# Performance work log

Measured on AMD Instinct MI355X. Metric: run time of the kernel, lower is better.

## Reference

```python
import jax, jax.numpy as jnp
import numpy as np

EPS = 1e-06

def phi(x):
    # canonical linear-attention feature map: elu(x) + 1 (positive features)
    return jax.nn.elu(x) + 1.0

def setup_inputs() -> dict:
    key = jax.random.key(0)
    kq, kk, kv = jax.random.split(key, 3)
    B, H, S, D = 4, 16, 4096, 64
    query = jax.random.normal(kq, (B, H, S, D), dtype=jnp.float32)
    k = jax.random.normal(kk, (B, H, S, D), dtype=jnp.float32)
    value = jax.random.normal(kv, (B, H, S, D), dtype=jnp.float32)
    attention_mask = jnp.ones((B, S), dtype=jnp.float32)
    return {"query": query, "key": k, "value": value, "attention_mask": attention_mask}

def reference(query, key, value, attention_mask):
    B, H, S, D = query.shape
    q = query / jnp.sqrt(jnp.asarray(D, query.dtype))
    phi_q = phi(q)                                   # [b,h,n,d]
    phi_k = phi(key)                                 # [b,h,n,d]
    mask = attention_mask[:, None, :, None].astype(phi_k.dtype)  # [b,1,n,1]
    phi_k = phi_k * mask
    kv_term = jnp.einsum('bhnd,bhnv->bhdv', phi_k, value)        # [b,h,d,v]
    output = jnp.einsum('bhnd,bhdv->bhnv', phi_q, kv_term)       # [b,h,n,v]
    k_one = jnp.sum(phi_k, axis=2)                               # [b,h,d] == phi_k @ masked ones
    normalizer = jnp.einsum('bhnd,bhd->bhn', phi_q, k_one)[..., None]  # [b,h,n,1]
    return output / (normalizer + EPS)
```

## Files before the change

kernel.cpp:

```cpp
#include <hip/hip_runtime.h>

#define NB 4
#define NH 16
#define NS 4096
#define ND 64
#define NBH (NB * NH)
#define EPSF 1e-6f

__device__ __forceinline__ float phi_f(float x) {
    return x > 0.0f ? x + 1.0f : __expf(x);
}

#define P1_CHUNK 512
#define P1_SUB 64

__global__ __launch_bounds__(256)
void la_pass1(const float* __restrict__ Kin, const float* __restrict__ Vin,
              const float* __restrict__ Min, float* __restrict__ KV,
              float* __restrict__ K1)
{
    const int tid = threadIdx.x;
    const int bh  = blockIdx.y;
    const int bb  = bh >> 4;
    const long long base = (long long)bh * NS * ND;
    const float* Kb = Kin + base;
    const float* Vb = Vin + base;
    const float* Mb = Min + (long long)bb * NS;

    __shared__ float sk[P1_SUB][ND];
    __shared__ float sv[P1_SUB][ND];

    const int lrow = tid >> 4;
    const int lcol = (tid & 15) * 4;
    const int d0 = (tid >> 4) * 4;
    const int v0 = (tid & 15) * 4;

    float acc[4][4];
    #pragma unroll
    for (int i = 0; i < 4; ++i)
        #pragma unroll
        for (int j = 0; j < 4; ++j) acc[i][j] = 0.0f;
    float acc1[4] = {0.f, 0.f, 0.f, 0.f};

    const int s0 = blockIdx.x * P1_CHUNK;
    const bool do_k1 = ((tid & 15) == 0);

    for (int t = 0; t < P1_CHUNK; t += P1_SUB) {
        __syncthreads();
        #pragma unroll
        for (int it = 0; it < 4; ++it) {
            const int r = lrow + 16 * it;
            const int srow = s0 + t + r;
            const float4 kq = *(const float4*)(Kb + (long long)srow * ND + lcol);
            const float4 vq = *(const float4*)(Vb + (long long)srow * ND + lcol);
            const float m = Mb[srow];
            float4 pk;
            pk.x = phi_f(kq.x) * m;
            pk.y = phi_f(kq.y) * m;
            pk.z = phi_f(kq.z) * m;
            pk.w = phi_f(kq.w) * m;
            *(float4*)(&sk[r][lcol]) = pk;
            *(float4*)(&sv[r][lcol]) = vq;
        }
        __syncthreads();
        #pragma unroll 4
        for (int r = 0; r < P1_SUB; ++r) {
            const float4 ka = *(const float4*)(&sk[r][d0]);
            const float4 vb = *(const float4*)(&sv[r][v0]);
            const float kav[4] = {ka.x, ka.y, ka.z, ka.w};
            const float vbv[4] = {vb.x, vb.y, vb.z, vb.w};
            #pragma unroll
            for (int i = 0; i < 4; ++i)
                #pragma unroll
                for (int j = 0; j < 4; ++j)
                    acc[i][j] += kav[i] * vbv[j];
            if (do_k1) {
                #pragma unroll
                for (int i = 0; i < 4; ++i) acc1[i] += kav[i];
            }
        }
    }

    float* kvb = KV + (long long)bh * ND * ND;
    #pragma unroll
    for (int i = 0; i < 4; ++i)
        #pragma unroll
        for (int j = 0; j < 4; ++j)
            atomicAdd(&kvb[(d0 + i) * ND + (v0 + j)], acc[i][j]);
    if (do_k1) {
        float* k1b = K1 + bh * ND;
        #pragma unroll
        for (int i = 0; i < 4; ++i) atomicAdd(&k1b[d0 + i], acc1[i]);
    }
}

#define P2_ROWS 128

__global__ __launch_bounds__(256)
void la_pass2(const float* __restrict__ Qin, const float* __restrict__ KV,
              const float* __restrict__ K1, float* __restrict__ Out)
{
    const int tid = threadIdx.x;
    const int bh  = blockIdx.y;
    const int s0  = blockIdx.x * P2_ROWS;
    const long long base = (long long)bh * NS * ND;

    __shared__ float sq[P2_ROWS][ND + 1];
    __shared__ float skv[ND][ND];
    __shared__ float sk1[ND];
    __shared__ float snorm[P2_ROWS];

    {
        const float4* kvsrc = (const float4*)(KV + (long long)bh * ND * ND);
        float4* kvdst = (float4*)(&skv[0][0]);
        #pragma unroll
        for (int i = 0; i < 4; ++i) kvdst[tid + 256 * i] = kvsrc[tid + 256 * i];
        if (tid < 16) ((float4*)sk1)[tid] = ((const float4*)(K1 + bh * ND))[tid];
    }

    {
        const int lrow = tid >> 4;
        const int lcol = (tid & 15) * 4;
        const float scale = 0.125f;
        #pragma unroll
        for (int it = 0; it < 8; ++it) {
            const int r = lrow + 16 * it;
            const float4 q4 = *(const float4*)(Qin + base + (long long)(s0 + r) * ND + lcol);
            sq[r][lcol + 0] = phi_f(q4.x * scale);
            sq[r][lcol + 1] = phi_f(q4.y * scale);
            sq[r][lcol + 2] = phi_f(q4.z * scale);
            sq[r][lcol + 3] = phi_f(q4.w * scale);
        }
    }
    __syncthreads();

    if (tid < P2_ROWS) {
        float n = 0.0f;
        #pragma unroll 8
        for (int d = 0; d < ND; ++d) n += sq[tid][d] * sk1[d];
        snorm[tid] = n;
    }
    __syncthreads();

    const int sg = tid >> 3;
    const int v0 = (tid & 7) * 8;
    const int r0 = sg * 4;

    float acc[4][8];
    #pragma unroll
    for (int j = 0; j < 4; ++j)
        #pragma unroll
        for (int k = 0; k < 8; ++k) acc[j][k] = 0.0f;

    #pragma unroll 4
    for (int d = 0; d < ND; ++d) {
        float q[4];
        #pragma unroll
        for (int j = 0; j < 4; ++j) q[j] = sq[r0 + j][d];
        const float4 b0 = *(const float4*)(&skv[d][v0]);
        const float4 b1 = *(const float4*)(&skv[d][v0 + 4]);
        const float bv[8] = {b0.x, b0.y, b0.z, b0.w, b1.x, b1.y, b1.z, b1.w};
        #pragma unroll
        for (int j = 0; j < 4; ++j)
            #pragma unroll
            for (int k = 0; k < 8; ++k)
                acc[j][k] += q[j] * bv[k];
    }

    float* outb = Out + base;
    #pragma unroll
    for (int j = 0; j < 4; ++j) {
        const int r = r0 + j;
        const float rn = 1.0f / (snorm[r] + EPSF);
        float4 o0, o1;
        o0.x = acc[j][0] * rn; o0.y = acc[j][1] * rn;
        o0.z = acc[j][2] * rn; o0.w = acc[j][3] * rn;
        o1.x = acc[j][4] * rn; o1.y = acc[j][5] * rn;
        o1.z = acc[j][6] * rn; o1.w = acc[j][7] * rn;
        *(float4*)(outb + (long long)(s0 + r) * ND + v0)     = o0;
        *(float4*)(outb + (long long)(s0 + r) * ND + v0 + 4) = o1;
    }
}

extern "C" void kernel_launch(void* const* d_in, const int* in_sizes, int n_in,
                              void* d_out, int out_size, void* d_ws, size_t ws_size,
                              hipStream_t stream)
{
    const float* Q = (const float*)d_in[0];
    const float* K = (const float*)d_in[1];
    const float* V = (const float*)d_in[2];
    const float* M = (const float*)d_in[3];
    float* Out = (float*)d_out;

    float* KV = (float*)d_ws;
    float* K1 = KV + (size_t)NBH * ND * ND;

    const size_t zbytes = ((size_t)NBH * ND * ND + (size_t)NBH * ND) * sizeof(float);
    hipMemsetAsync(d_ws, 0, zbytes, stream);

    dim3 g1(NS / P1_CHUNK, NBH);
    la_pass1<<<g1, dim3(256), 0, stream>>>(K, V, M, KV, K1);

    dim3 g2(NS / P2_ROWS, NBH);
    la_pass2<<<g2, dim3(256), 0, stream>>>(Q, KV, K1, Out);
}
```

Baseline: 256.4 us.

## Use single-wavefront blocks with 8x8 register tiles and register-prefetched loads

Both passes now run 64-thread blocks, one wavefront each, and every thread computes an 8x8 output tile instead of 4x4 or 4x8, which raises arithmetic per shared-memory load. Pass 1 uses smaller chunks and prefetches the next tile of K, V and the mask into registers while the current tile is being computed. Pass 2 transposes phi(Q) into shared memory so it can be read as float4, and it folds the normalizer dot product into the main loop. The trade-offs are many more blocks and many more atomics in pass 1, plus higher register pressure.

```diff
diff --git a/kernel.cpp b/kernel.cpp
--- a/kernel.cpp
+++ b/kernel.cpp
@@ -11,174 +11,220 @@
     return x > 0.0f ? x + 1.0f : __expf(x);
 }
 
-#define P1_CHUNK 512
-#define P1_SUB 64
-
-__global__ __launch_bounds__(256)
+#define P1_TILE 32
+#define P1_CHUNK 128
+
+__global__ __launch_bounds__(64)
 void la_pass1(const float* __restrict__ Kin, const float* __restrict__ Vin,
               const float* __restrict__ Min, float* __restrict__ KV,
               float* __restrict__ K1)
 {
-    const int tid = threadIdx.x;
-    const int bh  = blockIdx.y;
-    const int bb  = bh >> 4;
+    const int t  = threadIdx.x;
+    const int bh = blockIdx.y;
+    const int bb = bh >> 4;
     const long long base = (long long)bh * NS * ND;
     const float* Kb = Kin + base;
     const float* Vb = Vin + base;
     const float* Mb = Min + (long long)bb * NS;
 
-    __shared__ float sk[P1_SUB][ND];
-    __shared__ float sv[P1_SUB][ND];
-
-    const int lrow = tid >> 4;
-    const int lcol = (tid & 15) * 4;
-    const int d0 = (tid >> 4) * 4;
-    const int v0 = (tid & 15) * 4;
-
-    float acc[4][4];
-    #pragma unroll
-    for (int i = 0; i < 4; ++i)
-        #pragma unroll
-        for (int j = 0; j < 4; ++j) acc[i][j] = 0.0f;
-    float acc1[4] = {0.f, 0.f, 0.f, 0.f};
+    __shared__ float sk[P1_TILE * ND];
+    __shared__ float sv[P1_TILE * ND];
+
+    const int d0 = (t >> 3) * 8;
+    const int v0 = (t & 7) * 8;
+
+    float acc[8][8];
+    #pragma unroll
+    for (int i = 0; i < 8; ++i)
+        #pragma unroll
+        for (int j = 0; j < 8; ++j) acc[i][j] = 0.0f;
+    float acc1[8];
+    #pragma unroll
+    for (int i = 0; i < 8; ++i) acc1[i] = 0.0f;
 
     const int s0 = blockIdx.x * P1_CHUNK;
-    const bool do_k1 = ((tid & 15) == 0);
-
-    for (int t = 0; t < P1_CHUNK; t += P1_SUB) {
-        __syncthreads();
-        #pragma unroll
-        for (int it = 0; it < 4; ++it) {
-            const int r = lrow + 16 * it;
-            const int srow = s0 + t + r;
-            const float4 kq = *(const float4*)(Kb + (long long)srow * ND + lcol);
-            const float4 vq = *(const float4*)(Vb + (long long)srow * ND + lcol);
-            const float m = Mb[srow];
+
+    float4 kreg[8], vreg[8];
+    float  mreg[8];
+    #pragma unroll
+    for (int i = 0; i < 8; ++i) {
+        const int f = t + 64 * i;
+        const int r = f >> 4;
+        const int c = (f & 15) * 4;
+        const long long gr = (long long)(s0 + r) * ND + c;
+        kreg[i] = *(const float4*)(Kb + gr);
+        vreg[i] = *(const float4*)(Vb + gr);
+        mreg[i] = Mb[s0 + r];
+    }
+
+    for (int tile = 0; tile < P1_CHUNK / P1_TILE; ++tile) {
+        __syncthreads();
+        const int nt0 = s0 + (tile + 1) * P1_TILE;
+        #pragma unroll
+        for (int i = 0; i < 8; ++i) {
+            const int f = t + 64 * i;
             float4 pk;
-            pk.x = phi_f(kq.x) * m;
-            pk.y = phi_f(kq.y) * m;
-            pk.z = phi_f(kq.z) * m;
-            pk.w = phi_f(kq.w) * m;
-            *(float4*)(&sk[r][lcol]) = pk;
-            *(float4*)(&sv[r][lcol]) = vq;
+            pk.x = phi_f(kreg[i].x) * mreg[i];
+            pk.y = phi_f(kreg[i].y) * mreg[i];
+            pk.z = phi_f(kreg[i].z) * mreg[i];
+            pk.w = phi_f(kreg[i].w) * mreg[i];
+            *(float4*)(sk + f * 4) = pk;
+            *(float4*)(sv + f * 4) = vreg[i];
+            if (tile < P1_CHUNK / P1_TILE - 1) {
+                const int r = f >> 4;
+                const int c = (f & 15) * 4;
+                const long long gr = (long long)(nt0 + r) * ND + c;
+                kreg[i] = *(const float4*)(Kb + gr);
+                vreg[i] = *(const float4*)(Vb + gr);
+                mreg[i] = Mb[nt0 + r];
+            }
         }
         __syncthreads();
         #pragma unroll 4
-        for (int r = 0; r < P1_SUB; ++r) {
-            const float4 ka = *(const float4*)(&sk[r][d0]);
-            const float4 vb = *(const float4*)(&sv[r][v0]);
-            const float kav[4] = {ka.x, ka.y, ka.z, ka.w};
-            const float vbv[4] = {vb.x, vb.y, vb.z, vb.w};
+        for (int r = 0; r < P1_TILE; ++r) {
+            const float4 a0 = *(const float4*)(sk + r * ND + d0);
+            const float4 a1 = *(const float4*)(sk + r * ND + d0 + 4);
+            const float4 b0 = *(const float4*)(sv + r * ND + v0);
+            const float4 b1 = *(const float4*)(sv + r * ND + v0 + 4);
+            const float av[8] = {a0.x, a0.y, a0.z, a0.w, a1.x, a1.y, a1.z, a1.w};
+            const float bv[8] = {b0.x, b0.y, b0.z, b0.w, b1.x, b1.y, b1.z, b1.w};
             #pragma unroll
-            for (int i = 0; i < 4; ++i)
+            for (int i = 0; i < 8; ++i) {
+                acc1[i] += av[i];
                 #pragma unroll
-                for (int j = 0; j < 4; ++j)
-                    acc[i][j] += kav[i] * vbv[j];
-            if (do_k1) {
-                #pragma unroll
-                for (int i = 0; i < 4; ++i) acc1[i] += kav[i];
+                for (int j = 0; j < 8; ++j)
+                    acc[i][j] += av[i] * bv[j];
             }
         }
     }
 
     float* kvb = KV + (long long)bh * ND * ND;
     #pragma unroll
-    for (int i = 0; i < 4; ++i)
-        #pragma unroll
-        for (int j = 0; j < 4; ++j)
-            atomicAdd(&kvb[(d0 + i) * ND + (v0 + j)], acc[i][j]);
-    if (do_k1) {
+    for (int i = 0; i < 8; ++i)
+        #pragma unroll
+        for (int j = 0; j < 8; ++j)
+            atomicAdd(&kvb[(d0 + i) * ND + v0 + j], acc[i][j]);
+    if ((t & 7) == 0) {
         float* k1b = K1 + bh * ND;
         #pragma unroll
-        for (int i = 0; i < 4; ++i) atomicAdd(&k1b[d0 + i], acc1[i]);
-    }
-}
-
-#define P2_ROWS 128
-
-__global__ __launch_bounds__(256)
+        for (int i = 0; i < 8; ++i) atomicAdd(&k1b[d0 + i], acc1[i]);
+    }
+}
+
+#define P2_ROWS 64
+#define SQT_LD 68
+
+__global__ __launch_bounds__(64)
 void la_pass2(const float* __restrict__ Qin, const float* __restrict__ KV,
               const float* __restrict__ K1, float* __restrict__ Out)
 {
-    const int tid = threadIdx.x;
-    const int bh  = blockIdx.y;
-    const int s0  = blockIdx.x * P2_ROWS;
+    const int t  = threadIdx.x;
+    const int bh = blockIdx.y;
+    const int s0 = blockIdx.x * P2_ROWS;
     const long long base = (long long)bh * NS * ND;
 
-    __shared__ float sq[P2_ROWS][ND + 1];
-    __shared__ float skv[ND][ND];
+    __shared__ float skv[ND * ND];
+    __shared__ float sqT[ND * SQT_LD];
+    __shared__ float stmp[16 * 65];
     __shared__ float sk1[ND];
-    __shared__ float snorm[P2_ROWS];
-
+
+    float4 qld[16];
+    #pragma unroll
+    for (int q = 0; q < 4; ++q)
+        #pragma unroll
+        for (int i = 0; i < 4; ++i) {
+            const int f = t + 64 * i;
+            const int r = f >> 4;
+            const int c = (f & 15) * 4;
+            qld[q * 4 + i] = *(const float4*)(Qin + base + (long long)(s0 + 16 * q + r) * ND + c);
+        }
+    float4 kvld[16];
     {
-        const float4* kvsrc = (const float4*)(KV + (long long)bh * ND * ND);
-        float4* kvdst = (float4*)(&skv[0][0]);
-        #pragma unroll
-        for (int i = 0; i < 4; ++i) kvdst[tid + 256 * i] = kvsrc[tid + 256 * i];
-        if (tid < 16) ((float4*)sk1)[tid] = ((const float4*)(K1 + bh * ND))[tid];
-    }
+        const float4* src = (const float4*)(KV + (long long)bh * ND * ND);
+        #pragma unroll
+        for (int i = 0; i < 16; ++i) kvld[i] = src[t + 64 * i];
+    }
+    float4 k1ld;
+    if (t < 16) k1ld = ((const float4*)(K1 + bh * ND))[t];
 
     {
-        const int lrow = tid >> 4;
-        const int lcol = (tid & 15) * 4;
-        const float scale = 0.125f;
-        #pragma unroll
-        for (int it = 0; it < 8; ++it) {
-            const int r = lrow + 16 * it;
-            const float4 q4 = *(const float4*)(Qin + base + (long long)(s0 + r) * ND + lcol);
-            sq[r][lcol + 0] = phi_f(q4.x * scale);
-            sq[r][lcol + 1] = phi_f(q4.y * scale);
-            sq[r][lcol + 2] = phi_f(q4.z * scale);
-            sq[r][lcol + 3] = phi_f(q4.w * scale);
+        float4* dst = (float4*)skv;
+        #pragma unroll
+        for (int i = 0; i < 16; ++i) dst[t + 64 * i] = kvld[i];
+        if (t < 16) ((float4*)sk1)[t] = k1ld;
+    }
+
+    for (int q = 0; q < 4; ++q) {
+        __syncthreads();
+        #pragma unroll
+        for (int i = 0; i < 4; ++i) {
+            const int f = t + 64 * i;
+            const int r = f >> 4;
+            const int c = (f & 15) * 4;
+            const float4 v = qld[q * 4 + i];
+            stmp[r * 65 + c + 0] = phi_f(v.x * 0.125f);
+            stmp[r * 65 + c + 1] = phi_f(v.y * 0.125f);
+            stmp[r * 65 + c + 2] = phi_f(v.z * 0.125f);
+            stmp[r * 65 + c + 3] = phi_f(v.w * 0.125f);
+        }
+        __syncthreads();
+        float vals[16];
+        #pragma unroll
+        for (int rr = 0; rr < 16; ++rr) vals[rr] = stmp[rr * 65 + t];
+        #pragma unroll
+        for (int j = 0; j < 4; ++j) {
+            float4 w;
+            w.x = vals[4 * j + 0]; w.y = vals[4 * j + 1];
+            w.z = vals[4 * j + 2]; w.w = vals[4 * j + 3];
+            *(float4*)(sqT + t * SQT_LD + 16 * q + 4 * j) = w;
         }
     }
     __syncthreads();
 
-    if (tid < P2_ROWS) {
-        float n = 0.0f;
-        #pragma unroll 8
-        for (int d = 0; d < ND; ++d) n += sq[tid][d] * sk1[d];
-        snorm[tid] = n;
-    }
-    __syncthreads();
-
-    const int sg = tid >> 3;
-    const int v0 = (tid & 7) * 8;
-    const int r0 = sg * 4;
-
-    float acc[4][8];
-    #pragma unroll
-    for (int j = 0; j < 4; ++j)
-        #pragma unroll
-        for (int k = 0; k < 8; ++k) acc[j][k] = 0.0f;
-
-    #pragma unroll 4
-    for (int d = 0; d < ND; ++d) {
-        float q[4];
-        #pragma unroll
-        for (int j = 0; j < 4; ++j) q[j] = sq[r0 + j][d];
-        const float4 b0 = *(const float4*)(&skv[d][v0]);
-        const float4 b1 = *(const float4*)(&skv[d][v0 + 4]);
-        const float bv[8] = {b0.x, b0.y, b0.z, b0.w, b1.x, b1.y, b1.z, b1.w};
-        #pragma unroll
-        for (int j = 0; j < 4; ++j)
+    const int r0 = (t >> 3) * 8;
+    const int v0 = (t & 7) * 8;
+
+    float acc[8][8];
+    #pragma unroll
+    for (int i = 0; i < 8; ++i)
+        #pragma unroll
+        for (int j = 0; j < 8; ++j) acc[i][j] = 0.0f;
+    float nacc[8];
+    #pragma unroll
+    for (int i = 0; i < 8; ++i) nacc[i] = 0.0f;
+
+    for (int d = 0; d < ND; d += 4) {
+        const float4 s1 = *(const float4*)(sk1 + d);
+        const float s1v[4] = {s1.x, s1.y, s1.z, s1.w};
+        #pragma unroll
+        for (int k = 0; k < 4; ++k) {
+            const float4 q0 = *(const float4*)(sqT + (d + k) * SQT_LD + r0);
+            const float4 q1 = *(const float4*)(sqT + (d + k) * SQT_LD + r0 + 4);
+            const float4 b0 = *(const float4*)(skv + (d + k) * ND + v0);
+            const float4 b1 = *(const float4*)(skv + (d + k) * ND + v0 + 4);
+            const float qv[8] = {q0.x, q0.y, q0.z, q0.w, q1.x, q1.y, q1.z, q1.w};
+            const float bv[8] = {b0.x, b0.y, b0.z, b0.w, b1.x, b1.y, b1.z, b1.w};
             #pragma unroll
-            for (int k = 0; k < 8; ++k)
-                acc[j][k] += q[j] * bv[k];
+            for (int i = 0; i < 8; ++i) {
+                nacc[i] += qv[i] * s1v[k];
+                #pragma unroll
+                for (int j = 0; j < 8; ++j)
+                    acc[i][j] += qv[i] * bv[j];
+            }
+        }
     }
 
     float* outb = Out + base;
     #pragma unroll
-    for (int j = 0; j < 4; ++j) {
-        const int r = r0 + j;
-        const float rn = 1.0f / (snorm[r] + EPSF);
+    for (int i = 0; i < 8; ++i) {
+        const float rn = 1.0f / (nacc[i] + EPSF);
         float4 o0, o1;
-        o0.x = acc[j][0] * rn; o0.y = acc[j][1] * rn;
-        o0.z = acc[j][2] * rn; o0.w = acc[j][3] * rn;
-        o1.x = acc[j][4] * rn; o1.y = acc[j][5] * rn;
-        o1.z = acc[j][6] * rn; o1.w = acc[j][7] * rn;
-        *(float4*)(outb + (long long)(s0 + r) * ND + v0)     = o0;
-        *(float4*)(outb + (long long)(s0 + r) * ND + v0 + 4) = o1;
+        o0.x = acc[i][0] * rn; o0.y = acc[i][1] * rn;
+        o0.z = acc[i][2] * rn; o0.w = acc[i][3] * rn;
+        o1.x = acc[i][4] * rn; o1.y = acc[i][5] * rn;
+        o1.z = acc[i][6] * rn; o1.w = acc[i][7] * rn;
+        *(float4*)(outb + (long long)(s0 + r0 + i) * ND + v0)     = o0;
+        *(float4*)(outb + (long long)(s0 + r0 + i) * ND + v0 + 4) = o1;
     }
 }
 
@@ -199,8 +245,8 @@
     hipMemsetAsync(d_ws, 0, zbytes, stream);
 
     dim3 g1(NS / P1_CHUNK, NBH);
-    la_pass1<<<g1, dim3(256), 0, stream>>>(K, V, M, KV, K1);
+    la_pass1<<<g1, dim3(64), 0, stream>>>(K, V, M, KV, K1);
 
     dim3 g2(NS / P2_ROWS, NBH);
-    la_pass2<<<g2, dim3(256), 0, stream>>>(Q, KV, K1, Out);
-}
+    la_pass2<<<g2, dim3(64), 0, stream>>>(Q, KV, K1, Out);
+}
```

Measured after the change: 500.1 us. 95.1% more time.
